# Performance work log

Measured on AMD Instinct MI355X. Metric: run time of the kernel, lower is better.

## Reference

```python
import jax, jax.numpy as jnp
import numpy as np

D = 768      # hidden_size
L = 4        # num_hidden_layers
H = 12       # num_attention_heads
I = 3072     # intermediate_size
B, S = 2, 2048
EPS = 1e-5


def setup_inputs() -> dict:
    key = jax.random.key(0)
    ks = jax.random.split(key, 8)
    sc = 0.02
    return {
        "x": jax.random.normal(ks[0], (B, S, D), dtype=jnp.float32),
        # weights stored as [in, out] so y = x @ W + b (same math as torch Linear)
        "qkv_w": jax.random.normal(ks[1], (L, D, 3 * D), dtype=jnp.float32) * sc,
        "qkv_b": jnp.zeros((L, 3 * D), dtype=jnp.float32),
        "out_w": jax.random.normal(ks[2], (L, D, D), dtype=jnp.float32) * sc,
        "out_b": jnp.zeros((L, D), dtype=jnp.float32),
        "ln1_w": jnp.ones((L, D), dtype=jnp.float32),
        "ln1_b": jnp.zeros((L, D), dtype=jnp.float32),
        "fc1_w": jax.random.normal(ks[3], (L, D, I), dtype=jnp.float32) * sc,
        "fc1_b": jnp.zeros((L, I), dtype=jnp.float32),
        "fc2_w": jax.random.normal(ks[4], (L, I, D), dtype=jnp.float32) * sc,
        "fc2_b": jnp.zeros((L, D), dtype=jnp.float32),
        "ln2_w": jnp.ones((L, D), dtype=jnp.float32),
        "ln2_b": jnp.zeros((L, D), dtype=jnp.float32),
    }


def _layer_norm(x, w, b):
    mu = jnp.mean(x, axis=-1, keepdims=True)
    var = jnp.mean(jnp.square(x - mu), axis=-1, keepdims=True)
    return (x - mu) * jax.lax.rsqrt(var + EPS) * w + b


def _encoder(x, qkv_w, qkv_b, out_w, out_b, ln1_w, ln1_b,
             fc1_w, fc1_b, fc2_w, fc2_b, ln2_w, ln2_b):
    hd = D // H
    scale = 1.0 / jnp.sqrt(jnp.float32(hd))

    def block(x, p):
        (qw, qb, ow, ob, l1w, l1b, f1w, f1b, f2w, f2b, l2w, l2b) = p
        # --- attention sub-block (pre-norm residual) ---
        h = _layer_norm(x, l1w, l1b)
        qkv = h @ qw + qb                      # [B,S,3D]
        qkv = qkv.reshape(B, S, H, 3 * hd).transpose(0, 2, 1, 3)  # [B,H,S,3hd]
        q, k, v = jnp.split(qkv, 3, axis=-1)
        logits = jnp.einsum('bhqd,bhkd->bhqk', q, k) * scale       # [B,H,S,S]
        attn = jax.nn.softmax(logits, axis=-1)
        vals = jnp.einsum('bhqk,bhkd->bhqd', attn, v)              # [B,H,S,hd]
        vals = vals.transpose(0, 2, 1, 3).reshape(B, S, D)
        x = x + vals @ ow + ob
        # --- MLP sub-block (pre-norm residual) ---
        h = _layer_norm(x, l2w, l2b)
        h = jax.nn.gelu(h @ f1w + f1b, approximate=False)
        x = x + h @ f2w + f2b
        return x, None

    params = (qkv_w, qkv_b, out_w, out_b, ln1_w, ln1_b,
              fc1_w, fc1_b, fc2_w, fc2_b, ln2_w, ln2_b)
    x, _ = jax.lax.scan(block, x, params)
    return x


def reference(x, qkv_w, qkv_b, out_w, out_b, ln1_w, ln1_b,
              fc1_w, fc1_b, fc2_w, fc2_b, ln2_w, ln2_b):
    return _encoder(x, qkv_w, qkv_b, out_w, out_b, ln1_w, ln1_b,
                    fc1_w, fc1_b, fc2_w, fc2_b, ln2_w, ln2_b)
```

## Files before the change

### kernel.cpp

```cpp
#include <hip/hip_runtime.h>
#include <stdint.h>
#include <math.h>

#define D_MODEL 768
#define NTOK    4096
#define SEQ     2048
#define NHEAD   12
#define HDIM    64
#define D_FF    3072
#define QKV_N   2304

typedef unsigned short ushort_t;
typedef short  sh4    __attribute__((ext_vector_type(4)));
typedef short  short8 __attribute__((ext_vector_type(8)));
typedef float  f32x4  __attribute__((ext_vector_type(4)));
typedef float  f32x16 __attribute__((ext_vector_type(16)));

__device__ __forceinline__ float b2f(ushort_t u) {
  union { unsigned int u; float f; } v; v.u = ((unsigned int)u) << 16; return v.f;
}
__device__ __forceinline__ ushort_t f2b(float f) {
  union { float f; unsigned int u; } v; v.f = f;
  unsigned int u = v.u;
  return (ushort_t)((u + 0x7fffu + ((u >> 16) & 1u)) >> 16);
}
__device__ __forceinline__ unsigned cvtpk_bf16(float lo, float hi) {
  unsigned r;
  asm("v_cvt_pk_bf16_f32 %0, %1, %2" : "=v"(r) : "v"(lo), "v"(hi));
  return r;
}

__global__ __launch_bounds__(256) void transpose_layer(
    const float* __restrict__ qkv_w, const float* __restrict__ out_w,
    const float* __restrict__ fc1_w, const float* __restrict__ fc2_w,
    ushort_t* __restrict__ qkvT, ushort_t* __restrict__ outT,
    ushort_t* __restrict__ f1T, ushort_t* __restrict__ f2T) {
  __shared__ ushort_t tile[32][33];
  int bid = blockIdx.x;
  const float* src; ushort_t* dst; int K, N, tn, tk;
  if (bid < 1728)      { src = qkv_w; dst = qkvT; K = 768;  N = 2304; tn = bid % 72;  tk = bid / 72; }
  else if (bid < 2304) { int b = bid - 1728; src = out_w; dst = outT; K = 768;  N = 768;  tn = b % 24; tk = b / 24; }
  else if (bid < 4608) { int b = bid - 2304; src = fc1_w; dst = f1T;  K = 768;  N = 3072; tn = b % 96; tk = b / 96; }
  else                 { int b = bid - 4608; src = fc2_w; dst = f2T;  K = 3072; N = 768;  tn = b % 24; tk = b / 24; }
  int n0 = tn * 32, k0 = tk * 32;
  int tx = threadIdx.x, ty = threadIdx.y;
  #pragma unroll
  for (int i = 0; i < 32; i += 8)
    tile[ty + i][tx] = f2b(src[(size_t)(k0 + ty + i) * N + n0 + tx]);
  __syncthreads();
  #pragma unroll
  for (int i = 0; i < 32; i += 8)
    dst[(size_t)(n0 + ty + i) * K + k0 + tx] = tile[tx][ty + i];
}

__global__ __launch_bounds__(256) void ln_kernel(const float* __restrict__ x,
                                                 const float* __restrict__ w,
                                                 const float* __restrict__ b,
                                                 ushort_t* __restrict__ out) {
  __shared__ float red[4];
  int tok = blockIdx.x, t = threadIdx.x;
  const float* xr = x + (size_t)tok * D_MODEL;
  float v0 = xr[t], v1 = xr[t + 256], v2 = xr[t + 512];
  float s = v0 + v1 + v2;
  #pragma unroll
  for (int o = 1; o < 64; o <<= 1) s += __shfl_xor(s, o, 64);
  if ((t & 63) == 0) red[t >> 6] = s;
  __syncthreads();
  float mean = (red[0] + red[1] + red[2] + red[3]) * (1.0f / 768.0f);
  __syncthreads();
  float d0 = v0 - mean, d1 = v1 - mean, d2 = v2 - mean;
  float q = d0 * d0 + d1 * d1 + d2 * d2;
  #pragma unroll
  for (int o = 1; o < 64; o <<= 1) q += __shfl_xor(q, o, 64);
  if ((t & 63) == 0) red[t >> 6] = q;
  __syncthreads();
  float var = (red[0] + red[1] + red[2] + red[3]) * (1.0f / 768.0f);
  float rs = rsqrtf(var + 1e-5f);
  ushort_t* orow = out + (size_t)tok * D_MODEL;
  orow[t]       = f2b(d0 * rs * w[t]       + b[t]);
  orow[t + 256] = f2b(d1 * rs * w[t + 256] + b[t + 256]);
  orow[t + 512] = f2b(d2 * rs * w[t + 512] + b[t + 512]);
}

template <int EPI, int TN>
__global__ __launch_bounds__(256) void gemm_kernel(
    const ushort_t* __restrict__ A, const ushort_t* __restrict__ BT,
    const float* __restrict__ bias, const float* __restrict__ resid,
    float* __restrict__ Cf, ushort_t* __restrict__ Cb, int M, int N, int K) {
  constexpr int NI = (TN == 128) ? 4 : 2;
  __shared__ ushort_t As[2][128 * 32];
  __shared__ ushort_t Bs[2][TN * 32];
  int t = threadIdx.x;
  int lane = t & 63, wave = t >> 6;
  int m0 = blockIdx.y * 128, n0 = blockIdx.x * TN;
  int wm = (TN == 128) ? (wave & 1) * 64 : wave * 32;
  int wn = (TN == 128) ? (wave >> 1) * 64 : 0;
  int quad = lane >> 4, l16 = lane & 15;
  int kq = quad * 8;
  int lrow = lane >> 2, lcol = (lane & 3) * 8;

  auto stage = [&](int k0, int buf) {
    #pragma unroll
    for (int c = 0; c < 2; ++c) {
      int rowA = wave * 32 + c * 16 + lrow;
      const ushort_t* ga = A + (size_t)(m0 + rowA) * K + k0 + lcol;
      ushort_t* la = &As[buf][(wave * 32 + c * 16) * 32];
      __builtin_amdgcn_global_load_lds((const __attribute__((address_space(1))) void*)ga,
                                       (__attribute__((address_space(3))) void*)la, 16, 0, 0);
      if (TN == 128 || c == 0) {
        int rowB = (TN == 128) ? rowA : (wave * 16 + lrow);
        const ushort_t* gb = BT + (size_t)(n0 + rowB) * K + k0 + lcol;
        ushort_t* lb = (TN == 128) ? &Bs[buf][(wave * 32 + c * 16) * 32]
                                   : &Bs[buf][(wave * 16) * 32];
        __builtin_amdgcn_global_load_lds((const __attribute__((address_space(1))) void*)gb,
                                         (__attribute__((address_space(3))) void*)lb, 16, 0, 0);
      }
    }
  };

  f32x4 acc[NI][4];
  #pragma unroll
  for (int i = 0; i < NI; ++i)
    #pragma unroll
    for (int j = 0; j < 4; ++j) acc[i][j] = (f32x4){0.f, 0.f, 0.f, 0.f};

  stage(0, 0);
  int nk = K / 32;
  for (int ki = 0; ki < nk; ++ki) {
    int cur = ki & 1;
    __syncthreads();
    if (ki + 1 < nk) stage((ki + 1) * 32, cur ^ 1);
    short8 af[NI], bf[4];
    #pragma unroll
    for (int i = 0; i < NI; ++i)
      af[i] = *(const short8*)&As[cur][(wm + i * 16 + l16) * 32 + kq];
    #pragma unroll
    for (int j = 0; j < 4; ++j)
      bf[j] = *(const short8*)&Bs[cur][(wn + j * 16 + l16) * 32 + kq];
    #pragma unroll
    for (int i = 0; i < NI; ++i)
      #pragma unroll
      for (int j = 0; j < 4; ++j)
        acc[i][j] = __builtin_amdgcn_mfma_f32_16x16x32_bf16(af[i], bf[j], acc[i][j], 0, 0, 0);
  }

  #pragma unroll
  for (int i = 0; i < NI; ++i) {
    #pragma unroll
    for (int j = 0; j < 4; ++j) {
      int col = n0 + wn + j * 16 + l16;
      float bv = bias[col];
      #pragma unroll
      for (int r = 0; r < 4; ++r) {
        int row = m0 + wm + i * 16 + quad * 4 + r;
        float v = acc[i][j][r] + bv;
        if (EPI == 1) v = 0.5f * v * (1.0f + erff(v * 0.70710678118654752f));
        if (EPI == 2) v += resid[(size_t)row * N + col];
        if (EPI == 2) Cf[(size_t)row * N + col] = v;
        else          Cb[(size_t)row * N + col] = f2b(v);
      }
    }
  }
}

__global__ __launch_bounds__(256, 3) void attn_kernel(const ushort_t* __restrict__ qkv,
                                                      ushort_t* __restrict__ out) {
  __shared__ __align__(16) ushort_t Ks[2][64 * 72];
  __shared__ __align__(16) ushort_t Vt[2][64 * 72];
  int t = threadIdx.x;
  int lane = t & 63, wave = t >> 6;
  int l31 = lane & 31, h = lane >> 5, h8 = h * 8;
  int pair = wave >> 1;
  int wq = wave & 1;
  int qt = blockIdx.x;
  int bh = blockIdx.y;
  int b = bh / NHEAD, hd = bh % NHEAD;
  size_t base = (size_t)b * SEQ * QKV_N + hd * 192;

  const float kscale = 0.125f * 1.44269504088896f;

  short8 qf[4];
  {
    const ushort_t* qp = qkv + base + (size_t)(qt * 64 + wq * 32 + l31) * QKV_N + h8;
    #pragma unroll
    for (int ks = 0; ks < 4; ++ks) qf[ks] = *(const short8*)(qp + ks * 16);
  }

  int srow = t >> 2, scol = (t & 3) * 16;
  int vk = (t & 31) * 2, vd = (t >> 5) * 8;
  short8 krA[2], krB[2], vrA[2], vrB[2];
  auto kv_load = [&](int c, int p) {
    const ushort_t* gk = qkv + base + (size_t)(c * 64 + srow) * QKV_N + 64 + scol;
    krA[p] = *(const short8*)gk;
    krB[p] = *(const short8*)(gk + 8);
    const ushort_t* gv = qkv + base + (size_t)(c * 64 + vk) * QKV_N + 128 + vd;
    vrA[p] = *(const short8*)gv;
    vrB[p] = *(const short8*)(gv + QKV_N);
  };
  auto kv_write = [&](int p) {
    *(short8*)&Ks[p][srow * 72 + scol]     = krA[p];
    *(short8*)&Ks[p][srow * 72 + scol + 8] = krB[p];
    unsigned* vtw = (unsigned*)&Vt[p][0];
    #pragma unroll
    for (int e = 0; e < 8; ++e) {
      unsigned pk = (unsigned)(unsigned short)vrA[p][e] |
                    ((unsigned)(unsigned short)vrB[p][e] << 16);
      vtw[(vd + e) * 36 + (vk >> 1)] = pk;
    }
  };

  f32x16 o0, o1;
  #pragma unroll
  for (int i = 0; i < 16; ++i) { o0[i] = 0.f; o1[i] = 0.f; }
  float lsum = 0.f;

  kv_load(0, 0);
  kv_load(1, 1);
  for (int it = 0; it < SEQ / 128; ++it) {
    kv_write(0);
    kv_write(1);
    __syncthreads();
    if (it + 1 < SEQ / 128) {
      kv_load(2 * it + 2, 0);
      kv_load(2 * it + 3, 1);
    }

    f32x16 s0, s1;
    #pragma unroll
    for (int i = 0; i < 16; ++i) { s0[i] = 0.f; s1[i] = 0.f; }
    __builtin_amdgcn_s_setprio(1);
    #pragma unroll
    for (int ks = 0; ks < 4; ++ks) {
      short8 k0 = *(const short8*)&Ks[pair][(l31)      * 72 + ks * 16 + h8];
      short8 k1 = *(const short8*)&Ks[pair][(32 + l31) * 72 + ks * 16 + h8];
      s0 = __builtin_amdgcn_mfma_f32_32x32x16_bf16(k0, qf[ks], s0, 0, 0, 0);
      s1 = __builtin_amdgcn_mfma_f32_32x32x16_bf16(k1, qf[ks], s1, 0, 0, 0);
    }
    __builtin_amdgcn_s_setprio(0);

    unsigned wpk[2][4][2];
    #pragma unroll
    for (int t2 = 0; t2 < 2; ++t2) {
      #pragma unroll
      for (int g = 0; g < 4; ++g) {
        float p0, p1, p2, p3;
        if (t2 == 0) {
          p0 = exp2f(s0[4 * g + 0] * kscale); p1 = exp2f(s0[4 * g + 1] * kscale);
          p2 = exp2f(s0[4 * g + 2] * kscale); p3 = exp2f(s0[4 * g + 3] * kscale);
        } else {
          p0 = exp2f(s1[4 * g + 0] * kscale); p1 = exp2f(s1[4 * g + 1] * kscale);
          p2 = exp2f(s1[4 * g + 2] * kscale); p3 = exp2f(s1[4 * g + 3] * kscale);
        }
        lsum += (p0 + p1) + (p2 + p3);
        wpk[t2][g][0] = cvtpk_bf16(p0, p1);
        wpk[t2][g][1] = cvtpk_bf16(p2, p3);
      }
    }

    #pragma unroll
    for (int k4 = 0; k4 < 4; ++k4) {
      int t2 = k4 >> 1, j2 = (k4 & 1) * 2;
      unsigned frag[4];
      #pragma unroll
      for (int c = 0; c < 2; ++c) {
        unsigned a  = wpk[t2][j2][c];
        unsigned b2 = wpk[t2][j2 + 1][c];
        unsigned snd = h ? a : b2;
        unsigned rcv = (unsigned)__shfl_xor((int)snd, 32, 64);
        frag[c]     = h ? rcv : a;
        frag[2 + c] = h ? b2 : rcv;
      }
      union { unsigned u[4]; short8 s8; } uc;
      uc.u[0] = frag[0]; uc.u[1] = frag[1]; uc.u[2] = frag[2]; uc.u[3] = frag[3];
      short8 ap = uc.s8;
      short8 v0 = *(const short8*)&Vt[pair][(l31)      * 72 + k4 * 16 + h8];
      short8 v1 = *(const short8*)&Vt[pair][(32 + l31) * 72 + k4 * 16 + h8];
      __builtin_amdgcn_s_setprio(1);
      o0 = __builtin_amdgcn_mfma_f32_32x32x16_bf16(ap, v0, o0, 0, 0, 0);
      o1 = __builtin_amdgcn_mfma_f32_32x32x16_bf16(ap, v1, o1, 0, 0, 0);
      __builtin_amdgcn_s_setprio(0);
    }
    __syncthreads();
  }

  float* cb = (float*)&Ks[0][0];
  if (wave >= 2) {
    int slot = ((wave - 2) * 64 + lane) * 33;
    #pragma unroll
    for (int i = 0; i < 16; ++i) { cb[slot + i] = o0[i]; cb[slot + 16 + i] = o1[i]; }
    cb[slot + 32] = lsum;
  }
  __syncthreads();
  if (wave < 2) {
    int slot = (wave * 64 + lane) * 33;
    #pragma unroll
    for (int i = 0; i < 16; ++i) { o0[i] += cb[slot + i]; o1[i] += cb[slot + 16 + i]; }
    lsum += cb[slot + 32];
    lsum += __shfl_xor(lsum, 32, 64);

    size_t obase = (size_t)(b * SEQ + qt * 64 + wave * 32) * D_MODEL + hd * HDIM;
    #pragma unroll
    for (int g = 0; g < 4; ++g) {
      #pragma unroll
      for (int r = 0; r < 4; ++r) {
        int reg = 4 * g + r;
        int qrow = r + 8 * g + 4 * h;
        float inv = 1.0f / __shfl(lsum, qrow, 64);
        ushort_t* orow = out + obase + (size_t)qrow * D_MODEL;
        orow[l31]      = f2b(o0[reg] * inv);
        orow[32 + l31] = f2b(o1[reg] * inv);
      }
    }
  }
}

extern "C" void kernel_launch(void* const* d_in, const int* in_sizes, int n_in,
                              void* d_out, int out_size, void* d_ws, size_t ws_size,
                              hipStream_t stream) {
  const float* x_in  = (const float*)d_in[0];
  const float* qkv_w = (const float*)d_in[1];
  const float* qkv_b = (const float*)d_in[2];
  const float* out_w = (const float*)d_in[3];
  const float* out_b = (const float*)d_in[4];
  const float* ln1_w = (const float*)d_in[5];
  const float* ln1_b = (const float*)d_in[6];
  const float* fc1_w = (const float*)d_in[7];
  const float* fc1_b = (const float*)d_in[8];
  const float* fc2_w = (const float*)d_in[9];
  const float* fc2_b = (const float*)d_in[10];
  const float* ln2_w = (const float*)d_in[11];
  const float* ln2_b = (const float*)d_in[12];

  char* ws = (char*)d_ws;
  size_t off = 0;
  auto alloc = [&](size_t bytes) -> void* {
    void* p = ws + off; off += (bytes + 255) & ~(size_t)255; return p;
  };
  float*    buf_x  = (float*)   alloc((size_t)NTOK * D_MODEL * 4);
  float*    buf_x2 = (float*)   alloc((size_t)NTOK * D_MODEL * 4);
  ushort_t* bigb   = (ushort_t*)alloc((size_t)NTOK * D_FF * 2);
  ushort_t* h_b    = (ushort_t*)alloc((size_t)NTOK * D_MODEL * 2);
  ushort_t* at_b   = (ushort_t*)alloc((size_t)NTOK * D_MODEL * 2);
  ushort_t* qkvT   = (ushort_t*)alloc((size_t)QKV_N * D_MODEL * 2);
  ushort_t* outT   = (ushort_t*)alloc((size_t)D_MODEL * D_MODEL * 2);
  ushort_t* f1T    = (ushort_t*)alloc((size_t)D_FF * D_MODEL * 2);
  ushort_t* f2T    = (ushort_t*)alloc((size_t)D_MODEL * D_FF * 2);

  ushort_t* qkv_a = bigb;
  ushort_t* mlp_b = bigb;

  for (int l = 0; l < 4; ++l) {
    const float* resid_in = (l == 0) ? x_in : buf_x;
    transpose_layer<<<6912, dim3(32, 8), 0, stream>>>(
        qkv_w + (size_t)l * D_MODEL * QKV_N, out_w + (size_t)l * D_MODEL * D_MODEL,
        fc1_w + (size_t)l * D_MODEL * D_FF,  fc2_w + (size_t)l * D_FF * D_MODEL,
        qkvT, outT, f1T, f2T);
    ln_kernel<<<NTOK, 256, 0, stream>>>(resid_in, ln1_w + l * D_MODEL, ln1_b + l * D_MODEL, h_b);
    gemm_kernel<0, 128><<<dim3(QKV_N / 128, NTOK / 128), 256, 0, stream>>>(
        h_b, qkvT, qkv_b + l * QKV_N, nullptr, nullptr, qkv_a, NTOK, QKV_N, D_MODEL);
    attn_kernel<<<dim3(SEQ / 64, 2 * NHEAD), 256, 0, stream>>>(qkv_a, at_b);
    gemm_kernel<2, 64><<<dim3(D_MODEL / 64, NTOK / 128), 256, 0, stream>>>(
        at_b, outT, out_b + l * D_MODEL, resid_in, buf_x2, nullptr, NTOK, D_MODEL, D_MODEL);
    ln_kernel<<<NTOK, 256, 0, stream>>>(buf_x2, ln2_w + l * D_MODEL, ln2_b + l * D_MODEL, h_b);
    gemm_kernel<1, 128><<<dim3(D_FF / 128, NTOK / 128), 256, 0, stream>>>(
        h_b, f1T, fc1_b + l * D_FF, nullptr, nullptr, mlp_b, NTOK, D_FF, D_MODEL);
    float* x_next = (l < 3) ? buf_x : (float*)d_out;
    gemm_kernel<2, 64><<<dim3(D_MODEL / 64, NTOK / 128), 256, 0, stream>>>(
        mlp_b, f2T, fc2_b + l * D_MODEL, buf_x2, x_next, nullptr, NTOK, D_MODEL, D_FF);
  }
  (void)in_sizes; (void)n_in; (void)out_size; (void)ws_size;
}
```

Baseline: 987.6 us.

## Restructure attention waves to split keys, share K fragments, remap blocks per XCD

Each of the four attention waves now handles all 64 queries of the tile against its own 32-key slice of a 128-key chunk. Each K fragment is loaded once and reused for two query halves, and V is stored transposed in a single wider padded buffer. The cross-wave reduction at the end becomes a two-stage LDS exchange. Both the GEMM and attention kernels also remap block IDs so consecutive tiles land on the same XCD, aiming for better L2 locality. In exchange the kernel holds four output accumulators per wave instead of two, raising register pressure at 3 blocks per CU, and the epilogue gains extra barriers.

Measured after the change: 1.346 ms. +36.3%, slower.

```diff
diff --git a/kernel.cpp b/kernel.cpp
--- a/kernel.cpp
+++ b/kernel.cpp
@@ -11,7 +11,6 @@
 #define QKV_N   2304
 
 typedef unsigned short ushort_t;
-typedef short  sh4    __attribute__((ext_vector_type(4)));
 typedef short  short8 __attribute__((ext_vector_type(8)));
 typedef float  f32x4  __attribute__((ext_vector_type(4)));
 typedef float  f32x16 __attribute__((ext_vector_type(16)));
@@ -92,7 +91,13 @@
   __shared__ ushort_t Bs[2][TN * 32];
   int t = threadIdx.x;
   int lane = t & 63, wave = t >> 6;
-  int m0 = blockIdx.y * 128, n0 = blockIdx.x * TN;
+  int gx = gridDim.x;
+  int nwg = gx * gridDim.y;
+  int bid0 = blockIdx.y * gx + blockIdx.x;
+  int qn = nwg >> 3, rm = nwg & 7;
+  int xcd = bid0 & 7, pos = bid0 >> 3;
+  int wg = (xcd < rm ? xcd * (qn + 1) : rm * (qn + 1) + (xcd - rm) * qn) + pos;
+  int m0 = (wg / gx) * 128, n0 = (wg % gx) * TN;
   int wm = (TN == 128) ? (wave & 1) * 64 : wave * 32;
   int wn = (TN == 128) ? (wave >> 1) * 64 : 0;
   int quad = lane >> 4, l16 = lane & 15;
@@ -163,67 +168,70 @@
   }
 }
 
+#define KPAD 136
 __global__ __launch_bounds__(256, 3) void attn_kernel(const ushort_t* __restrict__ qkv,
                                                       ushort_t* __restrict__ out) {
-  __shared__ __align__(16) ushort_t Ks[2][64 * 72];
-  __shared__ __align__(16) ushort_t Vt[2][64 * 72];
+  __shared__ __align__(16) ushort_t smem[128 * 72 + 64 * KPAD];
+  ushort_t* Ks = smem;
+  ushort_t* Vt = smem + 128 * 72;
   int t = threadIdx.x;
   int lane = t & 63, wave = t >> 6;
   int l31 = lane & 31, h = lane >> 5, h8 = h * 8;
-  int pair = wave >> 1;
-  int wq = wave & 1;
-  int qt = blockIdx.x;
-  int bh = blockIdx.y;
+  int bid0 = blockIdx.y * 32 + blockIdx.x;
+  int wg = (bid0 & 7) * 96 + (bid0 >> 3);
+  int qt = wg & 31;
+  int bh = wg >> 5;
   int b = bh / NHEAD, hd = bh % NHEAD;
   size_t base = (size_t)b * SEQ * QKV_N + hd * 192;
+  int w32 = wave * 32;
 
   const float kscale = 0.125f * 1.44269504088896f;
 
-  short8 qf[4];
-  {
-    const ushort_t* qp = qkv + base + (size_t)(qt * 64 + wq * 32 + l31) * QKV_N + h8;
-    #pragma unroll
-    for (int ks = 0; ks < 4; ++ks) qf[ks] = *(const short8*)(qp + ks * 16);
-  }
-
-  int srow = t >> 2, scol = (t & 3) * 16;
-  int vk = (t & 31) * 2, vd = (t >> 5) * 8;
-  short8 krA[2], krB[2], vrA[2], vrB[2];
-  auto kv_load = [&](int c, int p) {
-    const ushort_t* gk = qkv + base + (size_t)(c * 64 + srow) * QKV_N + 64 + scol;
-    krA[p] = *(const short8*)gk;
-    krB[p] = *(const short8*)(gk + 8);
-    const ushort_t* gv = qkv + base + (size_t)(c * 64 + vk) * QKV_N + 128 + vd;
-    vrA[p] = *(const short8*)gv;
-    vrB[p] = *(const short8*)(gv + QKV_N);
+  short8 qf[2][4];
+  #pragma unroll
+  for (int qh = 0; qh < 2; ++qh) {
+    const ushort_t* qp = qkv + base + (size_t)(qt * 64 + qh * 32 + l31) * QKV_N + h8;
+    #pragma unroll
+    for (int ks = 0; ks < 4; ++ks) qf[qh][ks] = *(const short8*)(qp + ks * 16);
+  }
+
+  int krow = t >> 1, kcol = (t & 1) * 32;
+  int kp = t & 63, vdb = (t >> 6) * 16;
+  short8 kr[4], va[2], vb[2];
+  auto kv_load = [&](int sbase) {
+    const ushort_t* gk = qkv + base + (size_t)(sbase + krow) * QKV_N + 64 + kcol;
+    #pragma unroll
+    for (int i = 0; i < 4; ++i) kr[i] = *(const short8*)(gk + i * 8);
+    const ushort_t* gv = qkv + base + (size_t)(sbase + 2 * kp) * QKV_N + 128 + vdb;
+    va[0] = *(const short8*)gv;           va[1] = *(const short8*)(gv + 8);
+    vb[0] = *(const short8*)(gv + QKV_N); vb[1] = *(const short8*)(gv + QKV_N + 8);
   };
-  auto kv_write = [&](int p) {
-    *(short8*)&Ks[p][srow * 72 + scol]     = krA[p];
-    *(short8*)&Ks[p][srow * 72 + scol + 8] = krB[p];
-    unsigned* vtw = (unsigned*)&Vt[p][0];
-    #pragma unroll
-    for (int e = 0; e < 8; ++e) {
-      unsigned pk = (unsigned)(unsigned short)vrA[p][e] |
-                    ((unsigned)(unsigned short)vrB[p][e] << 16);
-      vtw[(vd + e) * 36 + (vk >> 1)] = pk;
-    }
+  auto kv_write = [&]() {
+    #pragma unroll
+    for (int i = 0; i < 4; ++i)
+      *(short8*)&Ks[krow * 72 + kcol + i * 8] = kr[i];
+    unsigned* vtw = (unsigned*)&Vt[0];
+    #pragma unroll
+    for (int half = 0; half < 2; ++half)
+      #pragma unroll
+      for (int e = 0; e < 8; ++e) {
+        unsigned pk = (unsigned)(unsigned short)va[half][e] |
+                      ((unsigned)(unsigned short)vb[half][e] << 16);
+        vtw[(vdb + half * 8 + e) * (KPAD / 2) + kp] = pk;
+      }
+    (void)0;
   };
 
-  f32x16 o0, o1;
-  #pragma unroll
-  for (int i = 0; i < 16; ++i) { o0[i] = 0.f; o1[i] = 0.f; }
-  float lsum = 0.f;
-
-  kv_load(0, 0);
-  kv_load(1, 1);
+  f32x16 o00, o01, o10, o11;
+  #pragma unroll
+  for (int i = 0; i < 16; ++i) { o00[i] = 0.f; o01[i] = 0.f; o10[i] = 0.f; o11[i] = 0.f; }
+  float ls0 = 0.f, ls1 = 0.f;
+
+  kv_load(0);
   for (int it = 0; it < SEQ / 128; ++it) {
-    kv_write(0);
-    kv_write(1);
+    kv_write();
     __syncthreads();
-    if (it + 1 < SEQ / 128) {
-      kv_load(2 * it + 2, 0);
-      kv_load(2 * it + 3, 1);
-    }
+    if (it + 1 < SEQ / 128) kv_load((it + 1) * 128);
 
     f32x16 s0, s1;
     #pragma unroll
@@ -231,84 +239,119 @@
     __builtin_amdgcn_s_setprio(1);
     #pragma unroll
     for (int ks = 0; ks < 4; ++ks) {
-      short8 k0 = *(const short8*)&Ks[pair][(l31)      * 72 + ks * 16 + h8];
-      short8 k1 = *(const short8*)&Ks[pair][(32 + l31) * 72 + ks * 16 + h8];
-      s0 = __builtin_amdgcn_mfma_f32_32x32x16_bf16(k0, qf[ks], s0, 0, 0, 0);
-      s1 = __builtin_amdgcn_mfma_f32_32x32x16_bf16(k1, qf[ks], s1, 0, 0, 0);
+      short8 kf = *(const short8*)&Ks[(w32 + l31) * 72 + ks * 16 + h8];
+      s0 = __builtin_amdgcn_mfma_f32_32x32x16_bf16(kf, qf[0][ks], s0, 0, 0, 0);
+      s1 = __builtin_amdgcn_mfma_f32_32x32x16_bf16(kf, qf[1][ks], s1, 0, 0, 0);
     }
     __builtin_amdgcn_s_setprio(0);
 
-    unsigned wpk[2][4][2];
-    #pragma unroll
-    for (int t2 = 0; t2 < 2; ++t2) {
-      #pragma unroll
-      for (int g = 0; g < 4; ++g) {
-        float p0, p1, p2, p3;
-        if (t2 == 0) {
-          p0 = exp2f(s0[4 * g + 0] * kscale); p1 = exp2f(s0[4 * g + 1] * kscale);
-          p2 = exp2f(s0[4 * g + 2] * kscale); p3 = exp2f(s0[4 * g + 3] * kscale);
-        } else {
-          p0 = exp2f(s1[4 * g + 0] * kscale); p1 = exp2f(s1[4 * g + 1] * kscale);
-          p2 = exp2f(s1[4 * g + 2] * kscale); p3 = exp2f(s1[4 * g + 3] * kscale);
-        }
-        lsum += (p0 + p1) + (p2 + p3);
-        wpk[t2][g][0] = cvtpk_bf16(p0, p1);
-        wpk[t2][g][1] = cvtpk_bf16(p2, p3);
+    unsigned wpk0[4][2], wpk1[4][2];
+    #pragma unroll
+    for (int g = 0; g < 4; ++g) {
+      float p0 = exp2f(s0[4 * g + 0] * kscale), p1 = exp2f(s0[4 * g + 1] * kscale);
+      float p2 = exp2f(s0[4 * g + 2] * kscale), p3 = exp2f(s0[4 * g + 3] * kscale);
+      ls0 += (p0 + p1) + (p2 + p3);
+      wpk0[g][0] = cvtpk_bf16(p0, p1);
+      wpk0[g][1] = cvtpk_bf16(p2, p3);
+    }
+    #pragma unroll
+    for (int g = 0; g < 4; ++g) {
+      float p0 = exp2f(s1[4 * g + 0] * kscale), p1 = exp2f(s1[4 * g + 1] * kscale);
+      float p2 = exp2f(s1[4 * g + 2] * kscale), p3 = exp2f(s1[4 * g + 3] * kscale);
+      ls1 += (p0 + p1) + (p2 + p3);
+      wpk1[g][0] = cvtpk_bf16(p0, p1);
+      wpk1[g][1] = cvtpk_bf16(p2, p3);
+    }
+
+    #pragma unroll
+    for (int k4 = 0; k4 < 2; ++k4) {
+      int j2 = k4 * 2;
+      unsigned f0[4], f1[4];
+      #pragma unroll
+      for (int c = 0; c < 2; ++c) {
+        unsigned a0 = wpk0[j2][c], b0 = wpk0[j2 + 1][c];
+        unsigned s0w = h ? a0 : b0;
+        unsigned r0 = (unsigned)__shfl_xor((int)s0w, 32, 64);
+        f0[c] = h ? r0 : a0;  f0[2 + c] = h ? b0 : r0;
+        unsigned a1 = wpk1[j2][c], b1 = wpk1[j2 + 1][c];
+        unsigned s1w = h ? a1 : b1;
+        unsigned r1 = (unsigned)__shfl_xor((int)s1w, 32, 64);
+        f1[c] = h ? r1 : a1;  f1[2 + c] = h ? b1 : r1;
       }
-    }
-
-    #pragma unroll
-    for (int k4 = 0; k4 < 4; ++k4) {
-      int t2 = k4 >> 1, j2 = (k4 & 1) * 2;
-      unsigned frag[4];
-      #pragma unroll
-      for (int c = 0; c < 2; ++c) {
-        unsigned a  = wpk[t2][j2][c];
-        unsigned b2 = wpk[t2][j2 + 1][c];
-        unsigned snd = h ? a : b2;
-        unsigned rcv = (unsigned)__shfl_xor((int)snd, 32, 64);
-        frag[c]     = h ? rcv : a;
-        frag[2 + c] = h ? b2 : rcv;
-      }
-      union { unsigned u[4]; short8 s8; } uc;
-      uc.u[0] = frag[0]; uc.u[1] = frag[1]; uc.u[2] = frag[2]; uc.u[3] = frag[3];
-      short8 ap = uc.s8;
-      short8 v0 = *(const short8*)&Vt[pair][(l31)      * 72 + k4 * 16 + h8];
-      short8 v1 = *(const short8*)&Vt[pair][(32 + l31) * 72 + k4 * 16 + h8];
+      union { unsigned u[4]; short8 s8; } u0, u1;
+      u0.u[0] = f0[0]; u0.u[1] = f0[1]; u0.u[2] = f0[2]; u0.u[3] = f0[3];
+      u1.u[0] = f1[0]; u1.u[1] = f1[1]; u1.u[2] = f1[2]; u1.u[3] = f1[3];
+      short8 ap0 = u0.s8, ap1 = u1.s8;
+      short8 v0 = *(const short8*)&Vt[(size_t)(l31)      * KPAD + w32 + k4 * 16 + h8];
+      short8 v1 = *(const short8*)&Vt[(size_t)(32 + l31) * KPAD + w32 + k4 * 16 + h8];
       __builtin_amdgcn_s_setprio(1);
-      o0 = __builtin_amdgcn_mfma_f32_32x32x16_bf16(ap, v0, o0, 0, 0, 0);
-      o1 = __builtin_amdgcn_mfma_f32_32x32x16_bf16(ap, v1, o1, 0, 0, 0);
+      o00 = __builtin_amdgcn_mfma_f32_32x32x16_bf16(ap0, v0, o00, 0, 0, 0);
+      o01 = __builtin_amdgcn_mfma_f32_32x32x16_bf16(ap0, v1, o01, 0, 0, 0);
+      o10 = __builtin_amdgcn_mfma_f32_32x32x16_bf16(ap1, v0, o10, 0, 0, 0);
+      o11 = __builtin_amdgcn_mfma_f32_32x32x16_bf16(ap1, v1, o11, 0, 0, 0);
       __builtin_amdgcn_s_setprio(0);
     }
     __syncthreads();
   }
 
-  float* cb = (float*)&Ks[0][0];
+  ls0 += __shfl_xor(ls0, 32, 64);
+  ls1 += __shfl_xor(ls1, 32, 64);
+
+  float* slab = (float*)&smem[0];
   if (wave >= 2) {
-    int slot = ((wave - 2) * 64 + lane) * 33;
-    #pragma unroll
-    for (int i = 0; i < 16; ++i) { cb[slot + i] = o0[i]; cb[slot + 16 + i] = o1[i]; }
-    cb[slot + 32] = lsum;
+    float* s = slab + (size_t)((wave - 2) * 64 + lane) * 68;
+    #pragma unroll
+    for (int i = 0; i < 16; ++i) {
+      s[i] = o00[i]; s[16 + i] = o01[i]; s[32 + i] = o10[i]; s[48 + i] = o11[i];
+    }
+    s[64] = ls0; s[65] = ls1;
   }
   __syncthreads();
   if (wave < 2) {
-    int slot = (wave * 64 + lane) * 33;
-    #pragma unroll
-    for (int i = 0; i < 16; ++i) { o0[i] += cb[slot + i]; o1[i] += cb[slot + 16 + i]; }
-    lsum += cb[slot + 32];
-    lsum += __shfl_xor(lsum, 32, 64);
-
-    size_t obase = (size_t)(b * SEQ + qt * 64 + wave * 32) * D_MODEL + hd * HDIM;
+    float* s = slab + (size_t)(wave * 64 + lane) * 68;
+    #pragma unroll
+    for (int i = 0; i < 16; ++i) {
+      o00[i] += s[i]; o01[i] += s[16 + i]; o10[i] += s[32 + i]; o11[i] += s[48 + i];
+    }
+    ls0 += s[64]; ls1 += s[65];
+  }
+  __syncthreads();
+  if (wave == 1) {
+    float* s = slab + (size_t)lane * 36;
+    #pragma unroll
+    for (int i = 0; i < 16; ++i) { s[i] = o00[i]; s[16 + i] = o01[i]; }
+    s[32] = ls0;
+  }
+  if (wave == 0) {
+    float* s = slab + (size_t)(64 + lane) * 36;
+    #pragma unroll
+    for (int i = 0; i < 16; ++i) { s[i] = o10[i]; s[16 + i] = o11[i]; }
+    s[32] = ls1;
+  }
+  __syncthreads();
+  if (wave < 2) {
+    float* s = slab + (size_t)(wave == 0 ? lane : 64 + lane) * 36;
+    f32x16 pa, pb; float lsf;
+    if (wave == 0) {
+      #pragma unroll
+      for (int i = 0; i < 16; ++i) { pa[i] = o00[i] + s[i]; pb[i] = o01[i] + s[16 + i]; }
+      lsf = ls0 + s[32];
+    } else {
+      #pragma unroll
+      for (int i = 0; i < 16; ++i) { pa[i] = o10[i] + s[i]; pb[i] = o11[i] + s[16 + i]; }
+      lsf = ls1 + s[32];
+    }
+    size_t ob = (size_t)(b * SEQ + qt * 64 + wave * 32) * D_MODEL + hd * HDIM;
     #pragma unroll
     for (int g = 0; g < 4; ++g) {
       #pragma unroll
       for (int r = 0; r < 4; ++r) {
         int reg = 4 * g + r;
-        int qrow = r + 8 * g + 4 * h;
-        float inv = 1.0f / __shfl(lsum, qrow, 64);
-        ushort_t* orow = out + obase + (size_t)qrow * D_MODEL;
-        orow[l31]      = f2b(o0[reg] * inv);
-        orow[32 + l31] = f2b(o1[reg] * inv);
+        int qrow = 8 * g + 4 * h + r;
+        float inv = 1.0f / __shfl(lsf, qrow, 64);
+        ushort_t* orow = out + ob + (size_t)qrow * D_MODEL;
+        orow[l31]      = f2b(pa[reg] * inv);
+        orow[32 + l31] = f2b(pb[reg] * inv);
       }
     }
   }
```
